# Optimization experiments

Hardware: AMD Instinct MI355X
Metric: run time of the kernel (lower is better)

The kernel has to match this reference:

```python
import jax, jax.numpy as jnp
import numpy as np

DECODING_TIME = 1.0
EPS = 1e-6


def setup_inputs() -> dict:
    key = jax.random.key(0)
    k1, k2, k3 = jax.random.split(key, 3)
    B, C, S = 1024, 100, 1000
    u = jax.random.normal(k1, (B, C), dtype=jnp.float32)
    # SPD covariance: cov = A A^T / C + 0.1 I
    A = jax.random.normal(k2, (B, C, C), dtype=jnp.float32)
    cov = jnp.einsum('bij,bkj->bik', A, A) / C + 0.1 * jnp.eye(C, dtype=jnp.float32)
    sample_point = jax.random.normal(k3, (S, C), dtype=jnp.float32)
    return {"u": u, "cov": cov, "sample_point": sample_point}


def reference(u, cov, sample_point):
    # Faithful translation of functional.gaussian_sampling_pred:
    # scale mean/cov by decoding time, regularize cov with eps*I,
    # batched Cholesky, affine-transform the standard-normal sample
    # points, softmax over classes, average over samples.
    C = u.shape[-1]
    scaled_u = u * DECODING_TIME                              # [B, C]
    scaled_cov = cov * DECODING_TIME + EPS * jnp.eye(C, dtype=cov.dtype)
    L = jnp.linalg.cholesky(scaled_cov)                       # [B, C, C]
    # samples = u + z @ L^T, z = sample_point  -> [B, S, C]
    samples = scaled_u[:, None, :] + jnp.einsum('sc,bdc->bsd', sample_point, L)
    probs = jax.nn.softmax(samples, axis=-1)                  # [B, S, C]
    pred = jnp.mean(probs, axis=1)                            # [B, C] (normalise=True)
    return pred
```

## Files before the change

kernel.cpp:

```cpp
#include <hip/hip_runtime.h>


#define CC    100
#define SS    1000
#define EPSF  1e-6f
#define NB    16
#define NDT   7
#define NCS   4
#define NST   63
#define LOG2E 1.44269504088896340736f

typedef short  s8 __attribute__((ext_vector_type(8)));
typedef float  f4 __attribute__((ext_vector_type(4)));

__device__ inline unsigned short f2bf(float x) {
    unsigned u = __float_as_uint(x);
    return (unsigned short)((u + 0x7fffu + ((u >> 16) & 1u)) >> 16);
}
__device__ inline float bf2f(unsigned short h) {
    return __uint_as_float(((unsigned)h) << 16);
}

__global__ __launch_bounds__(256)
void zconv_kernel(const float* __restrict__ z, unsigned short* __restrict__ zb) {
    const int stile = blockIdx.x;
    const int cs = threadIdx.x >> 6;
    const int l  = threadIdx.x & 63;
    const int s  = stile * 16 + (l & 15);
    const int c0 = cs * 32 + (l >> 4) * 8;
    unsigned short v[8];
    #pragma unroll
    for (int j = 0; j < 8; ++j) {
        const int c = c0 + j;
        float x = 0.0f;
        if (c < CC)      x = (s < SS) ? z[(size_t)s * CC + c] : 0.0f;
        else if (c <= CC + 1) x = 1.0f;
        v[j] = f2bf(x);
    }
    uint4 pk;
    pk.x = (unsigned)v[0] | ((unsigned)v[1] << 16);
    pk.y = (unsigned)v[2] | ((unsigned)v[3] << 16);
    pk.z = (unsigned)v[4] | ((unsigned)v[5] << 16);
    pk.w = (unsigned)v[6] | ((unsigned)v[7] << 16);
    reinterpret_cast<uint4*>(zb)[(stile * NCS + cs) * 64 + l] = pk;
}

template<int NPAN>
__device__ inline void panel_factor(float* __restrict__ M, int jb, int l) {
    float P0r[NPAN], P1r[NPAN];
    const int i1 = l + 64;
    #pragma unroll
    for (int jj = 0; jj < NPAN; ++jj) {
        P0r[jj] = M[(jb + jj) * CC + l];
        P1r[jj] = (i1 < CC) ? M[(jb + jj) * CC + i1] : 0.0f;
    }
    #pragma unroll
    for (int jj = 0; jj < NPAN; ++jj) {
        const int j = jb + jj;
        const float dsrc  = (j & 64) ? P1r[jj] : P0r[jj];
        const float val   = __shfl(dsrc, j & 63);
        const float dinv  = rsqrtf(val);
        const float s     = val * dinv;
        const float dinv2 = dinv * dinv;
        #pragma unroll
        for (int kk = jj + 1; kk < NPAN; ++kk) {
            const int k = jb + kk;
            const float tsrc = (k & 64) ? P1r[jj] : P0r[jj];
            const float t = __shfl(tsrc, k & 63) * dinv2;
            P0r[kk] -= P0r[jj] * t;
            P1r[kk] -= P1r[jj] * t;
        }
        P0r[jj] = (l == j) ? s : ((l > j) ? P0r[jj] * dinv : P0r[jj]);
        P1r[jj] = (i1 == j) ? s : ((i1 > j) ? P1r[jj] * dinv : P1r[jj]);
    }
    #pragma unroll
    for (int jj = 0; jj < NPAN; ++jj) {
        M[(jb + jj) * CC + l] = P0r[jj];
        if (i1 < CC) M[(jb + jj) * CC + i1] = P1r[jj];
    }
}

__global__ __launch_bounds__(256, 4)
void chol_kernel(const float* __restrict__ cov, const float* __restrict__ u,
                 unsigned short* __restrict__ Lb) {
    __shared__ float M[CC * CC];
    const int tid = threadIdx.x;
    const int w   = tid >> 6;
    const int l   = tid & 63;
    const int b   = blockIdx.x;

    const float4* c4 = reinterpret_cast<const float4*>(cov + (size_t)b * CC * CC);
    for (int t = tid; t < CC * CC / 4; t += 256)
        reinterpret_cast<float4*>(M)[t] = c4[t];
    __syncthreads();
    for (int d = tid; d < CC; d += 256) M[d * CC + d] += EPSF;
    __syncthreads();

    for (int jb = 0; jb < CC; jb += NB) {
        const int jend = (jb + NB < CC) ? jb + NB : CC;

        if (w == 0) {
            if (jend - jb == NB) panel_factor<NB>(M, jb, l);
            else                 panel_factor<CC - (CC / NB) * NB>(M, jb, l);
        }
        __syncthreads();

        if (jend < CC) {
            const int i0 = jend + l;
            const int i1 = i0 + 64;
            float P0[NB], P1[NB];
            #pragma unroll
            for (int jj = 0; jj < NB; ++jj) {
                P0[jj] = (i0 < CC) ? M[(jb + jj) * CC + i0] : 0.0f;
                P1[jj] = (i1 < CC) ? M[(jb + jj) * CC + i1] : 0.0f;
            }
            #pragma unroll 2
            for (int k = jend + w; k < CC; k += 4) {
                float bk[NB];
                #pragma unroll
                for (int jj = 0; jj < NB; ++jj)
                    bk[jj] = M[(jb + jj) * CC + k];
                if (i0 < CC) {
                    float acc = M[k * CC + i0];
                    #pragma unroll
                    for (int jj = 0; jj < NB; ++jj) acc -= P0[jj] * bk[jj];
                    M[k * CC + i0] = acc;
                }
                if (i1 < CC) {
                    float acc = M[k * CC + i1];
                    #pragma unroll
                    for (int jj = 0; jj < NB; ++jj) acc -= P1[jj] * bk[jj];
                    M[k * CC + i1] = acc;
                }
            }
        }
        __syncthreads();
    }

    const int tx = l & 15;
    const int ty = l >> 4;
    unsigned short* outp = Lb + (size_t)b * (NDT * NCS * 64 * 8);
    for (int f = w; f < NDT * NCS; f += 4) {
        const int dt = f >> 2, cs = f & 3;
        const int d  = dt * 16 + tx;
        const int c0 = cs * 32 + ty * 8;
        unsigned short v[8];
        #pragma unroll
        for (int j = 0; j < 8; ++j) {
            const int c = c0 + j;
            float x = 0.0f;
            if (c < CC) {
                if (d < CC && c <= d) x = M[c * CC + d] * LOG2E;
            } else if (c == CC) {
                if (d < CC) x = bf2f(f2bf(u[(size_t)b * CC + d] * LOG2E));
                else        x = -1e30f;
            } else if (c == CC + 1) {
                if (d < CC) {
                    const float t = u[(size_t)b * CC + d] * LOG2E;
                    x = t - bf2f(f2bf(t));
                }
            }
            v[j] = f2bf(x);
        }
        uint4 pk;
        pk.x = (unsigned)v[0] | ((unsigned)v[1] << 16);
        pk.y = (unsigned)v[2] | ((unsigned)v[3] << 16);
        pk.z = (unsigned)v[4] | ((unsigned)v[5] << 16);
        pk.w = (unsigned)v[6] | ((unsigned)v[7] << 16);
        reinterpret_cast<uint4*>(outp)[f * 64 + l] = pk;
    }
}

__global__ __launch_bounds__(256, 1)
void pred_kernel(const unsigned short* __restrict__ Lb,
                 const unsigned short* __restrict__ zb,
                 float* __restrict__ out) {
    __shared__ float red[4 * NDT * 16];
    const int tid = threadIdx.x, b = blockIdx.x;
    const int w  = tid >> 6;
    const int l  = tid & 63;
    const int li = l & 15;
    const int hi = l >> 4;

    s8 Bf[NDT][NCS];
    const s8* Lb8 = reinterpret_cast<const s8*>(Lb + (size_t)b * (NDT * NCS * 64 * 8));
    #pragma unroll
    for (int dt = 0; dt < NDT; ++dt)
        #pragma unroll
        for (int cs = 0; cs < NCS; ++cs)
            Bf[dt][cs] = Lb8[(dt * NCS + cs) * 64 + l];

    float meanAcc[NDT][4];
    #pragma unroll
    for (int dt = 0; dt < NDT; ++dt)
        #pragma unroll
        for (int r = 0; r < 4; ++r) meanAcc[dt][r] = 0.0f;

    const s8* zb8 = reinterpret_cast<const s8*>(zb);

    for (int st = w; st < NST; st += 4) {
        s8 Af[NCS];
        #pragma unroll
        for (int cs = 0; cs < NCS; ++cs)
            Af[cs] = zb8[(st * NCS + cs) * 64 + l];

        f4 acc[NDT];
        #pragma unroll
        for (int dt = 0; dt < NDT; ++dt) acc[dt] = (f4){0.f, 0.f, 0.f, 0.f};

        #pragma unroll
        for (int cs = 0; cs < NCS; ++cs)
            #pragma unroll
            for (int dt = 0; dt < NDT; ++dt)
                acc[dt] = __builtin_amdgcn_mfma_f32_16x16x32_bf16(
                              Bf[dt][cs], Af[cs], acc[dt], 0, 0, 0);

        float e[NDT][4];
        float rs = 0.0f;
        #pragma unroll
        for (int dt = 0; dt < NDT; ++dt)
            #pragma unroll
            for (int r = 0; r < 4; ++r) {
                const float ev = __builtin_amdgcn_exp2f(acc[dt][r]);
                e[dt][r] = ev;
                rs += ev;
            }
        rs += __shfl_xor(rs, 16);
        rs += __shfl_xor(rs, 32);
        const float wgt = (st * 16 + li < SS) ? __builtin_amdgcn_rcpf(rs) : 0.0f;
        #pragma unroll
        for (int dt = 0; dt < NDT; ++dt)
            #pragma unroll
            for (int r = 0; r < 4; ++r) meanAcc[dt][r] += e[dt][r] * wgt;
    }

    #pragma unroll
    for (int dt = 0; dt < NDT; ++dt)
        #pragma unroll
        for (int r = 0; r < 4; ++r) {
            float v = meanAcc[dt][r];
            v += __shfl_xor(v, 1);
            v += __shfl_xor(v, 2);
            v += __shfl_xor(v, 4);
            v += __shfl_xor(v, 8);
            if (li == 0) red[w * (NDT * 16) + dt * 16 + hi * 4 + r] = v;
        }
    __syncthreads();
    if (tid < CC) {
        const float sum = red[tid] + red[NDT * 16 + tid] +
                          red[2 * NDT * 16 + tid] + red[3 * NDT * 16 + tid];
        out[(size_t)b * CC + tid] = sum * (1.0f / (float)SS);
    }
}

extern "C" void kernel_launch(void* const* d_in, const int* in_sizes, int n_in,
                              void* d_out, int out_size, void* d_ws, size_t ws_size,
                              hipStream_t stream) {
    const float* u   = (const float*)d_in[0];
    const float* cov = (const float*)d_in[1];
    const float* z   = (const float*)d_in[2];
    float* outp = (float*)d_out;
    const int B = in_sizes[0] / CC;

    unsigned short* zb = (unsigned short*)d_ws;
    unsigned short* Lbf = (unsigned short*)((char*)d_ws + (1 << 20));

    zconv_kernel<<<dim3(NST), dim3(256), 0, stream>>>(z, zb);
    chol_kernel <<<dim3(B),   dim3(256), 0, stream>>>(cov, u, Lbf);
    pred_kernel <<<dim3(B),   dim3(256), 0, stream>>>(Lbf, zb, outp);
}
```

Baseline: 114.7 us.

## Use float2 column pairs and readlane broadcasts in Cholesky; split exp row-sum

Each lane now owns two adjacent columns stored as float2 instead of two columns 64 apart. This allows vectorized LDS loads and stores in the panel factorization and the trailing update. The trailing update now takes its bk coefficients from the panel registers through readlane broadcasts instead of re-reading them from LDS, and the unroll-2 pragma is dropped. The panel shuffles become readlanes, and the softmax row sum is split into two partial accumulators computed in place in acc. The readlane lane index depends on the loop variable k and must be wave-uniform, which risks extra scalar work or waterfall code.

```diff
diff --git a/kernel.cpp b/kernel.cpp
--- a/kernel.cpp
+++ b/kernel.cpp
@@ -20,6 +20,9 @@
 __device__ inline float bf2f(unsigned short h) {
     return __uint_as_float(((unsigned)h) << 16);
 }
+__device__ inline float lane_bcast(float x, int lane) {
+    return __int_as_float(__builtin_amdgcn_readlane(__float_as_int(x), lane));
+}
 
 __global__ __launch_bounds__(256)
 void zconv_kernel(const float* __restrict__ z, unsigned short* __restrict__ zb) {
@@ -47,37 +50,35 @@
 
 template<int NPAN>
 __device__ inline void panel_factor(float* __restrict__ M, int jb, int l) {
-    float P0r[NPAN], P1r[NPAN];
-    const int i1 = l + 64;
-    #pragma unroll
-    for (int jj = 0; jj < NPAN; ++jj) {
-        P0r[jj] = M[(jb + jj) * CC + l];
-        P1r[jj] = (i1 < CC) ? M[(jb + jj) * CC + i1] : 0.0f;
-    }
+    float2 P[NPAN];
+    const int c0 = 2 * l;
+    const bool vld = (c0 < CC);
+    #pragma unroll
+    for (int jj = 0; jj < NPAN; ++jj)
+        P[jj] = vld ? *reinterpret_cast<const float2*>(&M[(jb + jj) * CC + c0])
+                    : make_float2(0.f, 0.f);
     #pragma unroll
     for (int jj = 0; jj < NPAN; ++jj) {
         const int j = jb + jj;
-        const float dsrc  = (j & 64) ? P1r[jj] : P0r[jj];
-        const float val   = __shfl(dsrc, j & 63);
+        const float dsrc  = (j & 1) ? P[jj].y : P[jj].x;
+        const float val   = lane_bcast(dsrc, j >> 1);
         const float dinv  = rsqrtf(val);
         const float s     = val * dinv;
         const float dinv2 = dinv * dinv;
         #pragma unroll
         for (int kk = jj + 1; kk < NPAN; ++kk) {
             const int k = jb + kk;
-            const float tsrc = (k & 64) ? P1r[jj] : P0r[jj];
-            const float t = __shfl(tsrc, k & 63) * dinv2;
-            P0r[kk] -= P0r[jj] * t;
-            P1r[kk] -= P1r[jj] * t;
-        }
-        P0r[jj] = (l == j) ? s : ((l > j) ? P0r[jj] * dinv : P0r[jj]);
-        P1r[jj] = (i1 == j) ? s : ((i1 > j) ? P1r[jj] * dinv : P1r[jj]);
-    }
-    #pragma unroll
-    for (int jj = 0; jj < NPAN; ++jj) {
-        M[(jb + jj) * CC + l] = P0r[jj];
-        if (i1 < CC) M[(jb + jj) * CC + i1] = P1r[jj];
-    }
+            const float tsrc = (k & 1) ? P[jj].y : P[jj].x;
+            const float t = lane_bcast(tsrc, k >> 1) * dinv2;
+            P[kk].x -= P[jj].x * t;
+            P[kk].y -= P[jj].y * t;
+        }
+        P[jj].x = (c0 == j)     ? s : ((c0 > j)     ? P[jj].x * dinv : P[jj].x);
+        P[jj].y = (c0 + 1 == j) ? s : ((c0 + 1 > j) ? P[jj].y * dinv : P[jj].y);
+    }
+    #pragma unroll
+    for (int jj = 0; jj < NPAN; ++jj)
+        if (vld) *reinterpret_cast<float2*>(&M[(jb + jj) * CC + c0]) = P[jj];
 }
 
 __global__ __launch_bounds__(256, 4)
@@ -106,31 +107,29 @@
         __syncthreads();
 
         if (jend < CC) {
-            const int i0 = jend + l;
-            const int i1 = i0 + 64;
-            float P0[NB], P1[NB];
+            const int i0 = jend + 2 * l;
+            const bool vld = (i0 < CC);
+            float2 P[NB];
             #pragma unroll
-            for (int jj = 0; jj < NB; ++jj) {
-                P0[jj] = (i0 < CC) ? M[(jb + jj) * CC + i0] : 0.0f;
-                P1[jj] = (i1 < CC) ? M[(jb + jj) * CC + i1] : 0.0f;
-            }
-            #pragma unroll 2
+            for (int jj = 0; jj < NB; ++jj)
+                P[jj] = vld ? *reinterpret_cast<const float2*>(&M[(jb + jj) * CC + i0])
+                            : make_float2(0.f, 0.f);
             for (int k = jend + w; k < CC; k += 4) {
+                const int kr = k - jend;
                 float bk[NB];
                 #pragma unroll
-                for (int jj = 0; jj < NB; ++jj)
-                    bk[jj] = M[(jb + jj) * CC + k];
-                if (i0 < CC) {
-                    float acc = M[k * CC + i0];
+                for (int jj = 0; jj < NB; ++jj) {
+                    const float src = (kr & 1) ? P[jj].y : P[jj].x;
+                    bk[jj] = lane_bcast(src, kr >> 1);
+                }
+                if (vld) {
+                    float2 a = *reinterpret_cast<const float2*>(&M[k * CC + i0]);
                     #pragma unroll
-                    for (int jj = 0; jj < NB; ++jj) acc -= P0[jj] * bk[jj];
-                    M[k * CC + i0] = acc;
-                }
-                if (i1 < CC) {
-                    float acc = M[k * CC + i1];
-                    #pragma unroll
-                    for (int jj = 0; jj < NB; ++jj) acc -= P1[jj] * bk[jj];
-                    M[k * CC + i1] = acc;
+                    for (int jj = 0; jj < NB; ++jj) {
+                        a.x -= P[jj].x * bk[jj];
+                        a.y -= P[jj].y * bk[jj];
+                    }
+                    *reinterpret_cast<float2*>(&M[k * CC + i0]) = a;
                 }
             }
         }
@@ -215,23 +214,24 @@
                 acc[dt] = __builtin_amdgcn_mfma_f32_16x16x32_bf16(
                               Bf[dt][cs], Af[cs], acc[dt], 0, 0, 0);
 
-        float e[NDT][4];
-        float rs = 0.0f;
-        #pragma unroll
-        for (int dt = 0; dt < NDT; ++dt)
-            #pragma unroll
-            for (int r = 0; r < 4; ++r) {
-                const float ev = __builtin_amdgcn_exp2f(acc[dt][r]);
-                e[dt][r] = ev;
-                rs += ev;
-            }
+        float rs01 = 0.0f, rs23 = 0.0f;
+        #pragma unroll
+        for (int dt = 0; dt < NDT; ++dt) {
+            acc[dt][0] = __builtin_amdgcn_exp2f(acc[dt][0]);
+            acc[dt][1] = __builtin_amdgcn_exp2f(acc[dt][1]);
+            acc[dt][2] = __builtin_amdgcn_exp2f(acc[dt][2]);
+            acc[dt][3] = __builtin_amdgcn_exp2f(acc[dt][3]);
+            rs01 += acc[dt][0] + acc[dt][1];
+            rs23 += acc[dt][2] + acc[dt][3];
+        }
+        float rs = rs01 + rs23;
         rs += __shfl_xor(rs, 16);
         rs += __shfl_xor(rs, 32);
         const float wgt = (st * 16 + li < SS) ? __builtin_amdgcn_rcpf(rs) : 0.0f;
         #pragma unroll
         for (int dt = 0; dt < NDT; ++dt)
             #pragma unroll
-            for (int r = 0; r < 4; ++r) meanAcc[dt][r] += e[dt][r] * wgt;
+            for (int r = 0; r < 4; ++r) meanAcc[dt][r] += acc[dt][r] * wgt;
     }
 
     #pragma unroll
```

After: 155.9 us. 1.36x slower.

## Fuse Cholesky and prediction kernels into one per-batch kernel

Applied to the files above, without the earlier changes.

Merges chol_kernel and pred_kernel into a single gsp_kernel. The bf16 MFMA B-fragments are built straight from the factor in shared memory into registers, so they no longer go through a global workspace. The shared matrix buffer is reused for the final reduction, and the exp/sum loop is restructured to work in place on the accumulators. This removes a kernel launch and the global write/read of L, but the fused kernel has higher register pressure, runs under launch bounds of 2, and puts the serial Cholesky and the MFMA phase in the same block, which may reduce overlap across blocks.

```diff
diff --git a/kernel.cpp b/kernel.cpp
--- a/kernel.cpp
+++ b/kernel.cpp
@@ -80,14 +80,16 @@
     }
 }
 
-__global__ __launch_bounds__(256, 4)
-void chol_kernel(const float* __restrict__ cov, const float* __restrict__ u,
-                 unsigned short* __restrict__ Lb) {
-    __shared__ float M[CC * CC];
+__global__ __launch_bounds__(256, 2)
+void gsp_kernel(const float* __restrict__ cov, const float* __restrict__ u,
+                const unsigned short* __restrict__ zb, float* __restrict__ out) {
+    __shared__ alignas(16) float M[CC * CC];
     const int tid = threadIdx.x;
     const int w   = tid >> 6;
     const int l   = tid & 63;
     const int b   = blockIdx.x;
+    const int li  = l & 15;
+    const int hi  = l >> 4;
 
     const float4* c4 = reinterpret_cast<const float4*>(cov + (size_t)b * CC * CC);
     for (int t = tid; t < CC * CC / 4; t += 256)
@@ -137,58 +139,39 @@
         __syncthreads();
     }
 
-    const int tx = l & 15;
-    const int ty = l >> 4;
-    unsigned short* outp = Lb + (size_t)b * (NDT * NCS * 64 * 8);
-    for (int f = w; f < NDT * NCS; f += 4) {
-        const int dt = f >> 2, cs = f & 3;
-        const int d  = dt * 16 + tx;
-        const int c0 = cs * 32 + ty * 8;
-        unsigned short v[8];
-        #pragma unroll
-        for (int j = 0; j < 8; ++j) {
-            const int c = c0 + j;
-            float x = 0.0f;
-            if (c < CC) {
-                if (d < CC && c <= d) x = M[c * CC + d] * LOG2E;
-            } else if (c == CC) {
-                if (d < CC) x = bf2f(f2bf(u[(size_t)b * CC + d] * LOG2E));
-                else        x = -1e30f;
-            } else if (c == CC + 1) {
-                if (d < CC) {
-                    const float t = u[(size_t)b * CC + d] * LOG2E;
-                    x = t - bf2f(f2bf(t));
+    float uv[NDT], uhi[NDT];
+    #pragma unroll
+    for (int dt = 0; dt < NDT; ++dt) {
+        const int d = dt * 16 + li;
+        const float t = (d < CC) ? u[(size_t)b * CC + d] * LOG2E : 0.0f;
+        uv[dt]  = t;
+        uhi[dt] = bf2f(f2bf(t));
+    }
+    s8 Bf[NDT][NCS];
+    #pragma unroll
+    for (int dt = 0; dt < NDT; ++dt) {
+        const int d = dt * 16 + li;
+        #pragma unroll
+        for (int cs = 0; cs < NCS; ++cs) {
+            const int c0 = cs * 32 + hi * 8;
+            s8 r;
+            #pragma unroll
+            for (int j = 0; j < 8; ++j) {
+                const int c = c0 + j;
+                float x = 0.0f;
+                if (c < CC) {
+                    if (d < CC && c <= d) x = M[c * CC + d] * LOG2E;
+                } else if (c == CC) {
+                    x = (d < CC) ? uhi[dt] : -1e30f;
+                } else if (c == CC + 1) {
+                    if (d < CC) x = uv[dt] - uhi[dt];
                 }
+                r[j] = (short)f2bf(x);
             }
-            v[j] = f2bf(x);
-        }
-        uint4 pk;
-        pk.x = (unsigned)v[0] | ((unsigned)v[1] << 16);
-        pk.y = (unsigned)v[2] | ((unsigned)v[3] << 16);
-        pk.z = (unsigned)v[4] | ((unsigned)v[5] << 16);
-        pk.w = (unsigned)v[6] | ((unsigned)v[7] << 16);
-        reinterpret_cast<uint4*>(outp)[f * 64 + l] = pk;
-    }
-}
-
-__global__ __launch_bounds__(256, 1)
-void pred_kernel(const unsigned short* __restrict__ Lb,
-                 const unsigned short* __restrict__ zb,
-                 float* __restrict__ out) {
-    __shared__ float red[4 * NDT * 16];
-    const int tid = threadIdx.x, b = blockIdx.x;
-    const int w  = tid >> 6;
-    const int l  = tid & 63;
-    const int li = l & 15;
-    const int hi = l >> 4;
-
-    s8 Bf[NDT][NCS];
-    const s8* Lb8 = reinterpret_cast<const s8*>(Lb + (size_t)b * (NDT * NCS * 64 * 8));
-    #pragma unroll
-    for (int dt = 0; dt < NDT; ++dt)
-        #pragma unroll
-        for (int cs = 0; cs < NCS; ++cs)
-            Bf[dt][cs] = Lb8[(dt * NCS + cs) * 64 + l];
+            Bf[dt][cs] = r;
+        }
+    }
+    __syncthreads();
 
     float meanAcc[NDT][4];
     #pragma unroll
@@ -215,25 +198,27 @@
                 acc[dt] = __builtin_amdgcn_mfma_f32_16x16x32_bf16(
                               Bf[dt][cs], Af[cs], acc[dt], 0, 0, 0);
 
-        float e[NDT][4];
-        float rs = 0.0f;
-        #pragma unroll
-        for (int dt = 0; dt < NDT; ++dt)
-            #pragma unroll
-            for (int r = 0; r < 4; ++r) {
-                const float ev = __builtin_amdgcn_exp2f(acc[dt][r]);
-                e[dt][r] = ev;
-                rs += ev;
-            }
+        float rs01 = 0.0f, rs23 = 0.0f;
+        #pragma unroll
+        for (int dt = 0; dt < NDT; ++dt) {
+            acc[dt][0] = __builtin_amdgcn_exp2f(acc[dt][0]);
+            acc[dt][1] = __builtin_amdgcn_exp2f(acc[dt][1]);
+            acc[dt][2] = __builtin_amdgcn_exp2f(acc[dt][2]);
+            acc[dt][3] = __builtin_amdgcn_exp2f(acc[dt][3]);
+            rs01 += acc[dt][0] + acc[dt][1];
+            rs23 += acc[dt][2] + acc[dt][3];
+        }
+        float rs = rs01 + rs23;
         rs += __shfl_xor(rs, 16);
         rs += __shfl_xor(rs, 32);
         const float wgt = (st * 16 + li < SS) ? __builtin_amdgcn_rcpf(rs) : 0.0f;
         #pragma unroll
         for (int dt = 0; dt < NDT; ++dt)
             #pragma unroll
-            for (int r = 0; r < 4; ++r) meanAcc[dt][r] += e[dt][r] * wgt;
-    }
-
+            for (int r = 0; r < 4; ++r) meanAcc[dt][r] += acc[dt][r] * wgt;
+    }
+
+    float* red = M;
     #pragma unroll
     for (int dt = 0; dt < NDT; ++dt)
         #pragma unroll
@@ -263,9 +248,7 @@
     const int B = in_sizes[0] / CC;
 
     unsigned short* zb = (unsigned short*)d_ws;
-    unsigned short* Lbf = (unsigned short*)((char*)d_ws + (1 << 20));
 
     zconv_kernel<<<dim3(NST), dim3(256), 0, stream>>>(z, zb);
-    chol_kernel <<<dim3(B),   dim3(256), 0, stream>>>(cov, u, Lbf);
-    pred_kernel <<<dim3(B),   dim3(256), 0, stream>>>(Lbf, zb, outp);
-}
+    gsp_kernel  <<<dim3(B),   dim3(256), 0, stream>>>(cov, u, zb, outp);
+}
```

Result: slower. 138.5 us (+20.7%).

## Overlap Cholesky panel factorization with trailing update via lookahead

Applied to the files above, without the earlier changes.

Restructures the blocked Cholesky so the next panel's columns are updated first. Wave 0 then factors that panel while the other three waves update the rest of the trailing matrix, instead of three waves idling during each panel factorization. The softmax loop also reuses the MFMA accumulators in place and splits the row-sum into two partial accumulators to shorten dependency chains. This adds an extra barrier per block step and spreads the trailing update over only three waves.

```diff
diff --git a/kernel.cpp b/kernel.cpp
--- a/kernel.cpp
+++ b/kernel.cpp
@@ -80,6 +80,28 @@
     }
 }
 
+__device__ inline void trail_row(float* __restrict__ M, int jb, int k,
+                                 int i0, int i1,
+                                 const float* __restrict__ P0,
+                                 const float* __restrict__ P1) {
+    float bk[NB];
+    #pragma unroll
+    for (int jj = 0; jj < NB; ++jj)
+        bk[jj] = M[(jb + jj) * CC + k];
+    if (i0 < CC) {
+        float acc = M[k * CC + i0];
+        #pragma unroll
+        for (int jj = 0; jj < NB; ++jj) acc -= P0[jj] * bk[jj];
+        M[k * CC + i0] = acc;
+    }
+    if (i1 < CC) {
+        float acc = M[k * CC + i1];
+        #pragma unroll
+        for (int jj = 0; jj < NB; ++jj) acc -= P1[jj] * bk[jj];
+        M[k * CC + i1] = acc;
+    }
+}
+
 __global__ __launch_bounds__(256, 4)
 void chol_kernel(const float* __restrict__ cov, const float* __restrict__ u,
                  unsigned short* __restrict__ Lb) {
@@ -96,43 +118,33 @@
     for (int d = tid; d < CC; d += 256) M[d * CC + d] += EPSF;
     __syncthreads();
 
-    for (int jb = 0; jb < CC; jb += NB) {
-        const int jend = (jb + NB < CC) ? jb + NB : CC;
+    if (w == 0) panel_factor<NB>(M, 0, l);
+    __syncthreads();
+
+    for (int jb = 0; jb + NB < CC; jb += NB) {
+        const int jend = jb + NB;
+        const int nend = (jend + NB < CC) ? jend + NB : CC;
+
+        const int i0 = jend + l;
+        const int i1 = i0 + 64;
+        float P0[NB], P1[NB];
+        #pragma unroll
+        for (int jj = 0; jj < NB; ++jj) {
+            P0[jj] = (i0 < CC) ? M[(jb + jj) * CC + i0] : 0.0f;
+            P1[jj] = (i1 < CC) ? M[(jb + jj) * CC + i1] : 0.0f;
+        }
+
+        for (int k = jend + w; k < nend; k += 4)
+            trail_row(M, jb, k, i0, i1, P0, P1);
+        __syncthreads();
 
         if (w == 0) {
-            if (jend - jb == NB) panel_factor<NB>(M, jb, l);
-            else                 panel_factor<CC - (CC / NB) * NB>(M, jb, l);
-        }
-        __syncthreads();
-
-        if (jend < CC) {
-            const int i0 = jend + l;
-            const int i1 = i0 + 64;
-            float P0[NB], P1[NB];
-            #pragma unroll
-            for (int jj = 0; jj < NB; ++jj) {
-                P0[jj] = (i0 < CC) ? M[(jb + jj) * CC + i0] : 0.0f;
-                P1[jj] = (i1 < CC) ? M[(jb + jj) * CC + i1] : 0.0f;
-            }
+            if (nend - jend == NB) panel_factor<NB>(M, jend, l);
+            else                   panel_factor<CC - (CC / NB) * NB>(M, jend, l);
+        } else {
             #pragma unroll 2
-            for (int k = jend + w; k < CC; k += 4) {
-                float bk[NB];
-                #pragma unroll
-                for (int jj = 0; jj < NB; ++jj)
-                    bk[jj] = M[(jb + jj) * CC + k];
-                if (i0 < CC) {
-                    float acc = M[k * CC + i0];
-                    #pragma unroll
-                    for (int jj = 0; jj < NB; ++jj) acc -= P0[jj] * bk[jj];
-                    M[k * CC + i0] = acc;
-                }
-                if (i1 < CC) {
-                    float acc = M[k * CC + i1];
-                    #pragma unroll
-                    for (int jj = 0; jj < NB; ++jj) acc -= P1[jj] * bk[jj];
-                    M[k * CC + i1] = acc;
-                }
-            }
+            for (int k = nend + (w - 1); k < CC; k += 3)
+                trail_row(M, jb, k, i0, i1, P0, P1);
         }
         __syncthreads();
     }
@@ -215,23 +227,24 @@
                 acc[dt] = __builtin_amdgcn_mfma_f32_16x16x32_bf16(
                               Bf[dt][cs], Af[cs], acc[dt], 0, 0, 0);
 
-        float e[NDT][4];
-        float rs = 0.0f;
-        #pragma unroll
-        for (int dt = 0; dt < NDT; ++dt)
-            #pragma unroll
-            for (int r = 0; r < 4; ++r) {
-                const float ev = __builtin_amdgcn_exp2f(acc[dt][r]);
-                e[dt][r] = ev;
-                rs += ev;
-            }
+        float rs01 = 0.0f, rs23 = 0.0f;
+        #pragma unroll
+        for (int dt = 0; dt < NDT; ++dt) {
+            acc[dt][0] = __builtin_amdgcn_exp2f(acc[dt][0]);
+            acc[dt][1] = __builtin_amdgcn_exp2f(acc[dt][1]);
+            acc[dt][2] = __builtin_amdgcn_exp2f(acc[dt][2]);
+            acc[dt][3] = __builtin_amdgcn_exp2f(acc[dt][3]);
+            rs01 += acc[dt][0] + acc[dt][1];
+            rs23 += acc[dt][2] + acc[dt][3];
+        }
+        float rs = rs01 + rs23;
         rs += __shfl_xor(rs, 16);
         rs += __shfl_xor(rs, 32);
         const float wgt = (st * 16 + li < SS) ? __builtin_amdgcn_rcpf(rs) : 0.0f;
         #pragma unroll
         for (int dt = 0; dt < NDT; ++dt)
             #pragma unroll
-            for (int r = 0; r < 4; ++r) meanAcc[dt][r] += e[dt][r] * wgt;
+            for (int r = 0; r < 4; ++r) meanAcc[dt][r] += acc[dt][r] * wgt;
     }
 
     #pragma unroll
```

Result: slower. 117.4 us (+2.3%).
